# Optimization experiments

Measured on AMD Instinct MI355X. Metric: run time of the kernel, lower is better.

The kernel has to match this reference:

```python
import jax, jax.numpy as jnp
import numpy as np

BATCH = 2048
N = 2 * BATCH
TEMP = 0.5
BN_EPS = 1e-5
COS_EPS = 1e-8

# Precompute (constant) flat indices of the negative entries: all (i,j) with
# j != i and j != i +- BATCH. Each row has exactly N-2 negatives.
_mask = np.ones((N, N), dtype=bool)
np.fill_diagonal(_mask, False)
for _i in range(BATCH):
    _mask[_i, BATCH + _i] = False
    _mask[BATCH + _i, _i] = False
NEG_IDX = np.nonzero(_mask.reshape(-1))[0]  # (N*(N-2),)


def _projector(h, W1, gamma, beta, W2, b2):
    # Linear (no bias) -> BatchNorm1d (training-mode batch stats) -> ReLU -> Linear
    x = h @ W1.T                                   # (B, latent)
    mu = jnp.mean(x, axis=0)
    var = jnp.mean(jnp.square(x - mu), axis=0)     # biased var, as torch BN
    x = (x - mu) * jax.lax.rsqrt(var + BN_EPS) * gamma + beta
    x = jax.nn.relu(x)
    return x @ W2.T + b2                           # (B, proj)


def setup_inputs() -> dict:
    key = jax.random.key(0)
    ks = jax.random.split(key, 4)
    latent, proj = 2048, 256
    return {
        "h_i": jax.random.normal(ks[0], (BATCH, latent), jnp.float32),
        "h_j": jax.random.normal(ks[1], (BATCH, latent), jnp.float32),
        "W1": jax.random.normal(ks[2], (latent, latent), jnp.float32) / np.sqrt(latent),
        "gamma": jnp.ones((latent,), jnp.float32),
        "beta": jnp.zeros((latent,), jnp.float32),
        "W2": jax.random.normal(ks[3], (proj, latent), jnp.float32) / np.sqrt(latent),
        "b2": jnp.zeros((proj,), jnp.float32),
    }


def reference(h_i, h_j, W1, gamma, beta, W2, b2):
    z_i = _projector(h_i, W1, gamma, beta, W2, b2)
    z_j = _projector(h_j, W1, gamma, beta, W2, b2)
    z = jnp.concatenate([z_i, z_j], axis=0)                      # (N, proj)
    # cosine similarity: normalize once, then a single GEMM
    zn = z / jnp.maximum(jnp.linalg.norm(z, axis=1, keepdims=True), COS_EPS)
    sim = (zn @ zn.T) / TEMP                                     # (N, N)
    sim_i_j = jnp.diagonal(sim, offset=BATCH)                    # (BATCH,)
    sim_j_i = jnp.diagonal(sim, offset=-BATCH)                   # (BATCH,)
    positives = jnp.concatenate([sim_i_j, sim_j_i])[:, None]     # (N, 1)
    negatives = sim.reshape(-1)[NEG_IDX].reshape(N, N - 2)       # (N, N-2)
    logits = jnp.concatenate([positives, negatives], axis=1)     # (N, N-1)
    # cross-entropy with label 0 for every row, reduction='sum', then / N
    loss = jnp.sum(jax.nn.logsumexp(logits, axis=1) - logits[:, 0]) / N
    return loss
```

## Files before the change

### kernel.cpp

```cpp
#include <hip/hip_runtime.h>
#include <hip/hip_fp8.h>
#include <math.h>

#define BATCH   2048
#define NROWS   4096
#define LATENT  2048
#define PROJ    256
#define TEMP_INV 2.0f
#define BN_EPS  1e-5f
#define COS_EPS 1e-8f
#define W1SCALE 32.0f
#define W1INV   (1.0f / 32.0f)

typedef __bf16 bf16x8 __attribute__((ext_vector_type(8)));
typedef float  f32x4  __attribute__((ext_vector_type(4)));
typedef long   i64;

__device__ __forceinline__ unsigned short f2bf(float f) {
    union { float f; unsigned int u; } c; c.f = f;
    return (unsigned short)((c.u + 0x7FFFu + ((c.u >> 16) & 1u)) >> 16);
}
__device__ __forceinline__ float bf2f(unsigned short h) {
    union { unsigned int u; float f; } c; c.u = ((unsigned int)h) << 16;
    return c.f;
}
__device__ __forceinline__ unsigned char f2fp8(float f) {
    __hip_fp8_e4m3 t(f);
    return (unsigned char)t.__x;
}

__device__ __forceinline__ void gl_lds16(const void* g, void* l) {
    __builtin_amdgcn_global_load_lds(
        (const __attribute__((address_space(1))) void*)g,
        (__attribute__((address_space(3))) void*)l, 16, 0, 0);
}

__device__ __forceinline__ int swz(int R, int lk) {
    return R * 32 + ((lk ^ ((R >> 1) & 3)) << 3);
}
__device__ __forceinline__ int mix8(int R) {
    return (R & 7) ^ ((R >> 1) & 4);
}

#define G1 1048576
#define G2 2097152
#define G3 3145728
#define G4 3276800
__global__ __launch_bounds__(256) void cvt_all_kernel(
    const float* __restrict__ h_i, const float* __restrict__ h_j,
    const float* __restrict__ W1,  const float* __restrict__ W2,
    unsigned char* __restrict__ Hq, unsigned char* __restrict__ W1q,
    unsigned short* __restrict__ W2b)
{
    int i = blockIdx.x * 256 + threadIdx.x;
    if (i >= G4) return;
    if (i < G2) {
        const float* src = (i < G1) ? h_i : h_j;
        int off = (i < G1) ? i : i - G1;
        float4 v = reinterpret_cast<const float4*>(src)[off];
        uchar4 o;
        o.x = f2fp8(v.x); o.y = f2fp8(v.y); o.z = f2fp8(v.z); o.w = f2fp8(v.w);
        reinterpret_cast<uchar4*>(Hq)[i] = o;
    } else if (i < G3) {
        int off = i - G2;
        float4 v = reinterpret_cast<const float4*>(W1)[off];
        uchar4 o;
        o.x = f2fp8(v.x * W1SCALE); o.y = f2fp8(v.y * W1SCALE);
        o.z = f2fp8(v.z * W1SCALE); o.w = f2fp8(v.w * W1SCALE);
        reinterpret_cast<uchar4*>(W1q)[off] = o;
    } else {
        int off = i - G3;
        float4 v = reinterpret_cast<const float4*>(W2)[off];
        ushort4 o;
        o.x = f2bf(v.x); o.y = f2bf(v.y); o.z = f2bf(v.z); o.w = f2bf(v.w);
        reinterpret_cast<ushort4*>(W2b)[off] = o;
    }
}

template<int KSTRIDE, int KLEN, int WM, int WN>
__device__ __forceinline__ void mfma_loop(
    const unsigned short* __restrict__ Ab,
    const unsigned short* __restrict__ Bb,
    unsigned short* As, unsigned short* Bs,
    f32x4 acc[WM][WN], int tid)
{
    constexpr int BM = WM * 32;
    constexpr int BN = WN * 32;
    const int wid = tid >> 6, lane = tid & 63;
    const int mblk = (wid >> 1) * (WM * 16);
    const int nblk = (wid & 1) * (WN * 16);
    const int lr = lane & 15, lk = lane >> 4;
    for (int k0 = 0; k0 < KLEN; k0 += 32) {
        __syncthreads();
        #pragma unroll
        for (int u = 0; u < BM / 64; ++u) {
            int li = u * 256 + tid;
            int r = li >> 2, c = (li & 3) ^ ((li >> 3) & 3);
            gl_lds16(Ab + (size_t)r * KSTRIDE + k0 + c * 8, As + li * 8);
        }
        #pragma unroll
        for (int u = 0; u < BN / 64; ++u) {
            int li = u * 256 + tid;
            int r = li >> 2, c = (li & 3) ^ ((li >> 3) & 3);
            gl_lds16(Bb + (size_t)r * KSTRIDE + k0 + c * 8, Bs + li * 8);
        }
        __syncthreads();
        bf16x8 af[WM], bv[WN];
        #pragma unroll
        for (int i = 0; i < WM; ++i)
            af[i] = *reinterpret_cast<const bf16x8*>(As + swz(mblk + i * 16 + lr, lk));
        #pragma unroll
        for (int j = 0; j < WN; ++j)
            bv[j] = *reinterpret_cast<const bf16x8*>(Bs + swz(nblk + j * 16 + lr, lk));
        #pragma unroll
        for (int i = 0; i < WM; ++i)
            #pragma unroll
            for (int j = 0; j < WN; ++j)
                acc[i][j] = __builtin_amdgcn_mfma_f32_16x16x32_bf16(af[i], bv[j], acc[i][j], 0, 0, 0);
    }
}

__global__ __launch_bounds__(256, 4) void gemm1_fp8(
    const unsigned char* __restrict__ Hq, const unsigned char* __restrict__ W1q,
    unsigned short* __restrict__ Xb, float* __restrict__ sums, float* __restrict__ sumsqs)
{
    __shared__ __align__(16) unsigned char As[128 * 128];
    __shared__ __align__(16) unsigned char Bs[64 * 128];
    const int tid = threadIdx.x;
    const int m0 = blockIdx.y * 128, n0 = blockIdx.x * 64;
    const unsigned char* Ab = Hq + (size_t)m0 * LATENT;
    const unsigned char* Bb = W1q + (size_t)n0 * LATENT;
    const int wid = tid >> 6, lane = tid & 63;
    const int mblk = (wid >> 1) * 64, nblk = (wid & 1) * 32;
    const int lr = lane & 15, lk = lane >> 4;
    f32x4 zero = {0.f, 0.f, 0.f, 0.f};
    f32x4 acc[4][2];
    #pragma unroll
    for (int i = 0; i < 4; ++i) { acc[i][0] = zero; acc[i][1] = zero; }

    for (int k0 = 0; k0 < LATENT; k0 += 128) {
        __syncthreads();
        #pragma unroll
        for (int u = 0; u < 4; ++u) {
            int li = u * 256 + tid;
            int r = li >> 3, s = li & 7;
            gl_lds16(Ab + (size_t)r * LATENT + k0 + ((s ^ mix8(r)) * 16), As + li * 16);
        }
        #pragma unroll
        for (int u = 0; u < 2; ++u) {
            int li = u * 256 + tid;
            int r = li >> 3, s = li & 7;
            gl_lds16(Bb + (size_t)r * LATENT + k0 + ((s ^ mix8(r)) * 16), Bs + li * 16);
        }
        __syncthreads();
        i64 af[4][4], bv[2][4];
        #pragma unroll
        for (int i = 0; i < 4; ++i) {
            int R = mblk + i * 16 + lr;
            int mr = mix8(R);
            int base = R * 128 + (lk & 1) * 8;
            #pragma unroll
            for (int t = 0; t < 4; ++t) {
                int g = 2 * t + (lk >> 1);
                af[i][t] = *reinterpret_cast<const i64*>(As + base + ((g ^ mr) << 4));
            }
        }
        #pragma unroll
        for (int j = 0; j < 2; ++j) {
            int R = nblk + j * 16 + lr;
            int mr = mix8(R);
            int base = R * 128 + (lk & 1) * 8;
            #pragma unroll
            for (int t = 0; t < 4; ++t) {
                int g = 2 * t + (lk >> 1);
                bv[j][t] = *reinterpret_cast<const i64*>(Bs + base + ((g ^ mr) << 4));
            }
        }
        #pragma unroll
        for (int t = 0; t < 4; ++t)
            #pragma unroll
            for (int i = 0; i < 4; ++i)
                #pragma unroll
                for (int j = 0; j < 2; ++j)
                    acc[i][j] = __builtin_amdgcn_mfma_f32_16x16x32_fp8_fp8(
                        af[i][t], bv[j][t], acc[i][j], 0, 0, 0);
    }

    const int lq = lane >> 4;
    const int half = m0 >> 11;
    #pragma unroll
    for (int j = 0; j < 2; ++j) {
        float s = 0.f, q = 0.f;
        #pragma unroll
        for (int i = 0; i < 4; ++i)
            #pragma unroll
            for (int r = 0; r < 4; ++r) {
                float v = acc[i][j][r] * W1INV;
                s += v; q += v * v;
                int row = m0 + mblk + i * 16 + lq * 4 + r;
                int col = n0 + nblk + j * 16 + lr;
                Xb[(size_t)row * LATENT + col] = f2bf(v);
            }
        s += __shfl_xor(s, 16, 64);  q += __shfl_xor(q, 16, 64);
        s += __shfl_xor(s, 32, 64);  q += __shfl_xor(q, 32, 64);
        if (lq == 0) {
            int col = n0 + nblk + j * 16 + lr;
            atomicAdd(&sums[half * LATENT + col], s);
            atomicAdd(&sumsqs[half * LATENT + col], q);
        }
    }
}

__global__ __launch_bounds__(256) void gemm2_mfma(
    const unsigned short* __restrict__ Xb, const unsigned short* __restrict__ W2b,
    const float* __restrict__ sums, const float* __restrict__ sumsqs,
    const float* __restrict__ gamma, const float* __restrict__ beta,
    unsigned short* __restrict__ Zpb)
{
    __shared__ __align__(16) unsigned short As[128 * 32];
    __shared__ __align__(16) unsigned short Bs[64 * 32];
    __shared__ __align__(16) float scs[512];
    __shared__ __align__(16) float shs[512];
    const int tid = threadIdx.x;
    const int m0 = blockIdx.y * 128, n0 = blockIdx.x * 64, kc = blockIdx.z;
    const unsigned short* Ab = Xb + (size_t)m0 * LATENT + kc * 512;
    const unsigned short* Bb = W2b + (size_t)n0 * LATENT + kc * 512;
    const int half = m0 >> 11;
    #pragma unroll
    for (int u = 0; u < 2; ++u) {
        int e = u * 256 + tid;
        int col = kc * 512 + e;
        int g = half * LATENT + col;
        float mu  = sums[g] * (1.0f / BATCH);
        float var = sumsqs[g] * (1.0f / BATCH) - mu * mu;
        float sc = gamma[col] * rsqrtf(var + BN_EPS);
        scs[e] = sc;
        shs[e] = beta[col] - mu * sc;
    }
    const int wid = tid >> 6, lane = tid & 63;
    const int mblk = (wid >> 1) * 64, nblk = (wid & 1) * 32;
    const int lr = lane & 15, lk = lane >> 4;
    f32x4 zero = {0.f, 0.f, 0.f, 0.f};
    f32x4 acc[4][2];
    #pragma unroll
    for (int i = 0; i < 4; ++i) { acc[i][0] = zero; acc[i][1] = zero; }

    for (int k0 = 0; k0 < 512; k0 += 32) {
        __syncthreads();
        #pragma unroll
        for (int u = 0; u < 2; ++u) {
            int li = u * 256 + tid;
            int r = li >> 2, c = (li & 3) ^ ((li >> 3) & 3);
            gl_lds16(Ab + (size_t)r * LATENT + k0 + c * 8, As + li * 8);
        }
        {
            int li = tid;
            int r = li >> 2, c = (li & 3) ^ ((li >> 3) & 3);
            gl_lds16(Bb + (size_t)r * LATENT + k0 + c * 8, Bs + li * 8);
        }
        __syncthreads();
        float4 sc0 = *reinterpret_cast<const float4*>(scs + k0 + lk * 8);
        float4 sc1 = *reinterpret_cast<const float4*>(scs + k0 + lk * 8 + 4);
        float4 sh0 = *reinterpret_cast<const float4*>(shs + k0 + lk * 8);
        float4 sh1 = *reinterpret_cast<const float4*>(shs + k0 + lk * 8 + 4);
        bf16x8 af[4], bv[2];
        #pragma unroll
        for (int i = 0; i < 4; ++i) {
            bf16x8 raw = *reinterpret_cast<const bf16x8*>(As + swz(mblk + i * 16 + lr, lk));
            bf16x8 a;
            a[0] = (__bf16)fmaxf(fmaf((float)raw[0], sc0.x, sh0.x), 0.f);
            a[1] = (__bf16)fmaxf(fmaf((float)raw[1], sc0.y, sh0.y), 0.f);
            a[2] = (__bf16)fmaxf(fmaf((float)raw[2], sc0.z, sh0.z), 0.f);
            a[3] = (__bf16)fmaxf(fmaf((float)raw[3], sc0.w, sh0.w), 0.f);
            a[4] = (__bf16)fmaxf(fmaf((float)raw[4], sc1.x, sh1.x), 0.f);
            a[5] = (__bf16)fmaxf(fmaf((float)raw[5], sc1.y, sh1.y), 0.f);
            a[6] = (__bf16)fmaxf(fmaf((float)raw[6], sc1.z, sh1.z), 0.f);
            a[7] = (__bf16)fmaxf(fmaf((float)raw[7], sc1.w, sh1.w), 0.f);
            af[i] = a;
        }
        #pragma unroll
        for (int j = 0; j < 2; ++j)
            bv[j] = *reinterpret_cast<const bf16x8*>(Bs + swz(nblk + j * 16 + lr, lk));
        #pragma unroll
        for (int i = 0; i < 4; ++i)
            #pragma unroll
            for (int j = 0; j < 2; ++j)
                acc[i][j] = __builtin_amdgcn_mfma_f32_16x16x32_bf16(af[i], bv[j], acc[i][j], 0, 0, 0);
    }

    unsigned short* Zk = Zpb + (size_t)kc * NROWS * PROJ;
    const int lq = lane >> 4;
    #pragma unroll
    for (int i = 0; i < 4; ++i)
        #pragma unroll
        for (int j = 0; j < 2; ++j)
            #pragma unroll
            for (int r = 0; r < 4; ++r) {
                int row = m0 + mblk + i * 16 + lq * 4 + r;
                int col = n0 + nblk + j * 16 + lr;
                Zk[(size_t)row * PROJ + col] = f2bf(acc[i][j][r]);
            }
}

__global__ __launch_bounds__(256) void rownorm_kernel(
    const unsigned short* __restrict__ Zpb, const float* __restrict__ b2,
    unsigned short* __restrict__ ZNb)
{
    const int wave = threadIdx.x >> 6;
    const int lane = threadIdx.x & 63;
    const int row = blockIdx.x * 4 + wave;
    float v[4];
    float sq = 0.f;
    #pragma unroll
    for (int i = 0; i < 4; ++i) {
        int col = lane + i * 64;
        float t = b2[col];
        #pragma unroll
        for (int c = 0; c < 4; ++c)
            t += bf2f(Zpb[(size_t)c * NROWS * PROJ + (size_t)row * PROJ + col]);
        v[i] = t;
        sq += t * t;
    }
    #pragma unroll
    for (int off = 32; off > 0; off >>= 1) sq += __shfl_xor(sq, off, 64);
    float inv = 1.0f / fmaxf(sqrtf(sq), COS_EPS);
    #pragma unroll
    for (int i = 0; i < 4; ++i)
        ZNb[(size_t)row * PROJ + lane + i * 64] = f2bf(v[i] * inv);
}

__global__ __launch_bounds__(256) void simlse_mfma(
    const unsigned short* __restrict__ ZNb, float* __restrict__ rowsum,
    float* __restrict__ dgA, float* __restrict__ posA)
{
    if (blockIdx.x < blockIdx.y) return;
    __shared__ __align__(16) unsigned short As[128 * 32];
    __shared__ __align__(16) unsigned short Bs[128 * 32];
    const int tid = threadIdx.x;
    const int r0 = blockIdx.y * 128, j0 = blockIdx.x * 128;
    const bool offdiag = (j0 != r0);
    f32x4 zero = {0.f, 0.f, 0.f, 0.f};
    f32x4 acc[4][4];
    #pragma unroll
    for (int i = 0; i < 4; ++i)
        #pragma unroll
        for (int j = 0; j < 4; ++j) acc[i][j] = zero;
    mfma_loop<PROJ, PROJ, 4, 4>(ZNb + (size_t)r0 * PROJ, ZNb + (size_t)j0 * PROJ,
                                As, Bs, acc, tid);
    const int wid = tid >> 6, lane = tid & 63;
    const int mblk = (wid >> 1) * 64, nblk = (wid & 1) * 64;
    const int lr = lane & 15, lq = lane >> 4;
    float tcol[4] = {0.f, 0.f, 0.f, 0.f};
    #pragma unroll
    for (int i = 0; i < 4; ++i)
        #pragma unroll
        for (int r = 0; r < 4; ++r) {
            int R = r0 + mblk + i * 16 + lq * 4 + r;
            int P = (R < BATCH) ? R + BATCH : R - BATCH;
            float t = 0.f;
            #pragma unroll
            for (int j = 0; j < 4; ++j) {
                int J = j0 + nblk + j * 16 + lr;
                float s = acc[i][j][r] * TEMP_INV;
                float e = __expf(s);
                t += e;
                tcol[j] += e;
                if (J == R) dgA[R] = e;
                if (J == P) { posA[R] = s; posA[J] = s; }
            }
            t += __shfl_xor(t, 1, 64);
            t += __shfl_xor(t, 2, 64);
            t += __shfl_xor(t, 4, 64);
            t += __shfl_xor(t, 8, 64);
            if (lr == 0) atomicAdd(&rowsum[R], t);
        }
    if (offdiag) {
        #pragma unroll
        for (int j = 0; j < 4; ++j) {
            float c = tcol[j];
            c += __shfl_xor(c, 16, 64);
            c += __shfl_xor(c, 32, 64);
            if (lq == 0) atomicAdd(&rowsum[j0 + nblk + j * 16 + lr], c);
        }
    }
}

__global__ __launch_bounds__(256) void loss_kernel(
    const float* __restrict__ rowsum, const float* __restrict__ dgA,
    const float* __restrict__ posA, float* __restrict__ out)
{
    __shared__ float red[256];
    float s = 0.f;
    for (int r = threadIdx.x; r < NROWS; r += 256)
        s += logf(rowsum[r] - dgA[r]) - posA[r];
    red[threadIdx.x] = s;
    __syncthreads();
    for (int off = 128; off > 0; off >>= 1) {
        if (threadIdx.x < off) red[threadIdx.x] += red[threadIdx.x + off];
        __syncthreads();
    }
    if (threadIdx.x == 0) out[0] = red[0] * (1.0f / NROWS);
}

extern "C" void kernel_launch(void* const* d_in, const int* in_sizes, int n_in,
                              void* d_out, int out_size, void* d_ws, size_t ws_size,
                              hipStream_t stream)
{
    const float* h_i   = (const float*)d_in[0];
    const float* h_j   = (const float*)d_in[1];
    const float* W1    = (const float*)d_in[2];
    const float* gamma = (const float*)d_in[3];
    const float* beta  = (const float*)d_in[4];
    const float* W2    = (const float*)d_in[5];
    const float* b2    = (const float*)d_in[6];
    float* out = (float*)d_out;

    unsigned short* Zpb = (unsigned short*)d_ws;
    float* sums   = (float*)(Zpb + (size_t)4 * NROWS * PROJ);
    float* sumsqs = sums + 2 * LATENT;
    float* rowsum = sumsqs + 2 * LATENT;
    float* dgA    = rowsum + NROWS;
    float* posA   = dgA + NROWS;
    unsigned char* Hq  = (unsigned char*)(posA + NROWS);
    unsigned char* W1q = Hq + (size_t)NROWS * LATENT;
    unsigned short* W2b = (unsigned short*)(W1q + (size_t)LATENT * LATENT);
    unsigned short* Xb  = W2b + (size_t)PROJ * LATENT;
    unsigned short* ZNb = Xb + (size_t)NROWS * LATENT;

    hipMemsetAsync(sums, 0, (size_t)(4 * LATENT + NROWS) * sizeof(float), stream);

    cvt_all_kernel<<<(G4 + 255) / 256, 256, 0, stream>>>(h_i, h_j, W1, W2, Hq, W1q, W2b);
    gemm1_fp8<<<dim3(LATENT / 64, NROWS / 128), 256, 0, stream>>>(Hq, W1q, Xb, sums, sumsqs);
    gemm2_mfma<<<dim3(PROJ / 64, NROWS / 128, 4), 256, 0, stream>>>(Xb, W2b, sums, sumsqs, gamma, beta, Zpb);
    rownorm_kernel<<<NROWS / 4, 256, 0, stream>>>(Zpb, b2, ZNb);
    simlse_mfma<<<dim3(NROWS / 128, NROWS / 128), 256, 0, stream>>>(ZNb, rowsum, dgA, posA);
    loss_kernel<<<1, 256, 0, stream>>>(rowsum, dgA, posA, out);
}
```

Before: 176.0 us.

## Move projector second GEMM and similarity GEMM to FP8 MFMA

The hidden activations are stored as FP8 instead of BF16. BatchNorm+ReLU moves out of the GEMM2 inner loop into a separate in-place pass, and GEMM2 then runs on a shared FP8 MFMA loop with W2 quantized and scaled. The normalized embeddings are quantized to scaled FP8, and the similarity GEMM loads the full K=256 tile into LDS once and uses FP8 MFMA. The accumulator memset is folded into the conversion kernel. The aim is to halve operand bandwidth and raise MFMA throughput, at the cost of an extra elementwise pass and a loss of accuracy from FP8 rounding in the logits.

```diff
diff --git a/kernel.cpp b/kernel.cpp
--- a/kernel.cpp
+++ b/kernel.cpp
@@ -6,15 +6,15 @@
 #define NROWS   4096
 #define LATENT  2048
 #define PROJ    256
-#define TEMP_INV 2.0f
 #define BN_EPS  1e-5f
 #define COS_EPS 1e-8f
 #define W1SCALE 32.0f
 #define W1INV   (1.0f / 32.0f)
-
-typedef __bf16 bf16x8 __attribute__((ext_vector_type(8)));
-typedef float  f32x4  __attribute__((ext_vector_type(4)));
-typedef long   i64;
+#define ZNSCALE 16.0f
+#define SIMSCALE (1.0f / 128.0f)
+
+typedef float f32x4 __attribute__((ext_vector_type(4)));
+typedef long  i64;
 
 __device__ __forceinline__ unsigned short f2bf(float f) {
     union { float f; unsigned int u; } c; c.f = f;
@@ -27,6 +27,10 @@
 __device__ __forceinline__ unsigned char f2fp8(float f) {
     __hip_fp8_e4m3 t(f);
     return (unsigned char)t.__x;
+}
+__device__ __forceinline__ float fp82f(unsigned char b) {
+    __hip_fp8_e4m3 t; t.__x = b;
+    return (float)t;
 }
 
 __device__ __forceinline__ void gl_lds16(const void* g, void* l) {
@@ -35,9 +39,6 @@
         (__attribute__((address_space(3))) void*)l, 16, 0, 0);
 }
 
-__device__ __forceinline__ int swz(int R, int lk) {
-    return R * 32 + ((lk ^ ((R >> 1) & 3)) << 3);
-}
 __device__ __forceinline__ int mix8(int R) {
     return (R & 7) ^ ((R >> 1) & 4);
 }
@@ -50,9 +51,13 @@
     const float* __restrict__ h_i, const float* __restrict__ h_j,
     const float* __restrict__ W1,  const float* __restrict__ W2,
     unsigned char* __restrict__ Hq, unsigned char* __restrict__ W1q,
-    unsigned short* __restrict__ W2b)
+    unsigned char* __restrict__ W2q, float* __restrict__ zeroacc)
 {
     int i = blockIdx.x * 256 + threadIdx.x;
+    if (blockIdx.x == 0) {
+        #pragma unroll
+        for (int u = 0; u < 48; ++u) zeroacc[u * 256 + threadIdx.x] = 0.f;
+    }
     if (i >= G4) return;
     if (i < G2) {
         const float* src = (i < G1) ? h_i : h_j;
@@ -71,86 +76,34 @@
     } else {
         int off = i - G3;
         float4 v = reinterpret_cast<const float4*>(W2)[off];
-        ushort4 o;
-        o.x = f2bf(v.x); o.y = f2bf(v.y); o.z = f2bf(v.z); o.w = f2bf(v.w);
-        reinterpret_cast<ushort4*>(W2b)[off] = o;
-    }
-}
-
-template<int KSTRIDE, int KLEN, int WM, int WN>
-__device__ __forceinline__ void mfma_loop(
-    const unsigned short* __restrict__ Ab,
-    const unsigned short* __restrict__ Bb,
-    unsigned short* As, unsigned short* Bs,
-    f32x4 acc[WM][WN], int tid)
-{
-    constexpr int BM = WM * 32;
-    constexpr int BN = WN * 32;
-    const int wid = tid >> 6, lane = tid & 63;
-    const int mblk = (wid >> 1) * (WM * 16);
-    const int nblk = (wid & 1) * (WN * 16);
-    const int lr = lane & 15, lk = lane >> 4;
-    for (int k0 = 0; k0 < KLEN; k0 += 32) {
-        __syncthreads();
-        #pragma unroll
-        for (int u = 0; u < BM / 64; ++u) {
-            int li = u * 256 + tid;
-            int r = li >> 2, c = (li & 3) ^ ((li >> 3) & 3);
-            gl_lds16(Ab + (size_t)r * KSTRIDE + k0 + c * 8, As + li * 8);
-        }
-        #pragma unroll
-        for (int u = 0; u < BN / 64; ++u) {
-            int li = u * 256 + tid;
-            int r = li >> 2, c = (li & 3) ^ ((li >> 3) & 3);
-            gl_lds16(Bb + (size_t)r * KSTRIDE + k0 + c * 8, Bs + li * 8);
-        }
-        __syncthreads();
-        bf16x8 af[WM], bv[WN];
-        #pragma unroll
-        for (int i = 0; i < WM; ++i)
-            af[i] = *reinterpret_cast<const bf16x8*>(As + swz(mblk + i * 16 + lr, lk));
-        #pragma unroll
-        for (int j = 0; j < WN; ++j)
-            bv[j] = *reinterpret_cast<const bf16x8*>(Bs + swz(nblk + j * 16 + lr, lk));
-        #pragma unroll
-        for (int i = 0; i < WM; ++i)
-            #pragma unroll
-            for (int j = 0; j < WN; ++j)
-                acc[i][j] = __builtin_amdgcn_mfma_f32_16x16x32_bf16(af[i], bv[j], acc[i][j], 0, 0, 0);
-    }
-}
-
-__global__ __launch_bounds__(256, 4) void gemm1_fp8(
-    const unsigned char* __restrict__ Hq, const unsigned char* __restrict__ W1q,
-    unsigned short* __restrict__ Xb, float* __restrict__ sums, float* __restrict__ sumsqs)
-{
-    __shared__ __align__(16) unsigned char As[128 * 128];
-    __shared__ __align__(16) unsigned char Bs[64 * 128];
-    const int tid = threadIdx.x;
-    const int m0 = blockIdx.y * 128, n0 = blockIdx.x * 64;
-    const unsigned char* Ab = Hq + (size_t)m0 * LATENT;
-    const unsigned char* Bb = W1q + (size_t)n0 * LATENT;
+        uchar4 o;
+        o.x = f2fp8(v.x * W1SCALE); o.y = f2fp8(v.y * W1SCALE);
+        o.z = f2fp8(v.z * W1SCALE); o.w = f2fp8(v.w * W1SCALE);
+        reinterpret_cast<uchar4*>(W2q)[off] = o;
+    }
+}
+
+template<int KSTRIDE, int KLEN>
+__device__ __forceinline__ void fp8_loop(
+    const unsigned char* __restrict__ Ab, const unsigned char* __restrict__ Bb,
+    unsigned char* As, unsigned char* Bs, f32x4 acc[4][2], int tid)
+{
     const int wid = tid >> 6, lane = tid & 63;
     const int mblk = (wid >> 1) * 64, nblk = (wid & 1) * 32;
     const int lr = lane & 15, lk = lane >> 4;
-    f32x4 zero = {0.f, 0.f, 0.f, 0.f};
-    f32x4 acc[4][2];
-    #pragma unroll
-    for (int i = 0; i < 4; ++i) { acc[i][0] = zero; acc[i][1] = zero; }
-
-    for (int k0 = 0; k0 < LATENT; k0 += 128) {
+    for (int k0 = 0; k0 < KLEN; k0 += 128) {
         __syncthreads();
         #pragma unroll
         for (int u = 0; u < 4; ++u) {
             int li = u * 256 + tid;
             int r = li >> 3, s = li & 7;
-            gl_lds16(Ab + (size_t)r * LATENT + k0 + ((s ^ mix8(r)) * 16), As + li * 16);
+            gl_lds16(Ab + (size_t)r * KSTRIDE + k0 + ((s ^ mix8(r)) * 16), As + li * 16);
         }
         #pragma unroll
         for (int u = 0; u < 2; ++u) {
             int li = u * 256 + tid;
             int r = li >> 3, s = li & 7;
-            gl_lds16(Bb + (size_t)r * LATENT + k0 + ((s ^ mix8(r)) * 16), Bs + li * 16);
+            gl_lds16(Bb + (size_t)r * KSTRIDE + k0 + ((s ^ mix8(r)) * 16), Bs + li * 16);
         }
         __syncthreads();
         i64 af[4][4], bv[2][4];
@@ -185,8 +138,25 @@
                     acc[i][j] = __builtin_amdgcn_mfma_f32_16x16x32_fp8_fp8(
                         af[i][t], bv[j][t], acc[i][j], 0, 0, 0);
     }
-
-    const int lq = lane >> 4;
+}
+
+__global__ __launch_bounds__(256, 4) void gemm1_fp8(
+    const unsigned char* __restrict__ Hq, const unsigned char* __restrict__ W1q,
+    unsigned char* __restrict__ Xq, float* __restrict__ sums, float* __restrict__ sumsqs)
+{
+    __shared__ __align__(16) unsigned char As[128 * 128];
+    __shared__ __align__(16) unsigned char Bs[64 * 128];
+    const int tid = threadIdx.x;
+    const int m0 = blockIdx.y * 128, n0 = blockIdx.x * 64;
+    f32x4 zero = {0.f, 0.f, 0.f, 0.f};
+    f32x4 acc[4][2];
+    #pragma unroll
+    for (int i = 0; i < 4; ++i) { acc[i][0] = zero; acc[i][1] = zero; }
+    fp8_loop<LATENT, LATENT>(Hq + (size_t)m0 * LATENT, W1q + (size_t)n0 * LATENT,
+                             As, Bs, acc, tid);
+    const int wid = tid >> 6, lane = tid & 63;
+    const int mblk = (wid >> 1) * 64, nblk = (wid & 1) * 32;
+    const int lr = lane & 15, lq = lane >> 4;
     const int half = m0 >> 11;
     #pragma unroll
     for (int j = 0; j < 2; ++j) {
@@ -199,7 +169,7 @@
                 s += v; q += v * v;
                 int row = m0 + mblk + i * 16 + lq * 4 + r;
                 int col = n0 + nblk + j * 16 + lr;
-                Xb[(size_t)row * LATENT + col] = f2bf(v);
+                Xq[(size_t)row * LATENT + col] = f2fp8(v);
             }
         s += __shfl_xor(s, 16, 64);  q += __shfl_xor(q, 16, 64);
         s += __shfl_xor(s, 32, 64);  q += __shfl_xor(q, 32, 64);
@@ -211,85 +181,52 @@
     }
 }
 
-__global__ __launch_bounds__(256) void gemm2_mfma(
-    const unsigned short* __restrict__ Xb, const unsigned short* __restrict__ W2b,
-    const float* __restrict__ sums, const float* __restrict__ sumsqs,
-    const float* __restrict__ gamma, const float* __restrict__ beta,
+__global__ __launch_bounds__(256) void bnrelu8_kernel(
+    unsigned char* __restrict__ Xq, const float* __restrict__ sums,
+    const float* __restrict__ sumsqs, const float* __restrict__ gamma,
+    const float* __restrict__ beta)
+{
+    const int row = blockIdx.x;
+    const int half = row >> 11;
+    const int col = threadIdx.x * 8;
+    size_t idx = (size_t)row * LATENT + col;
+    uchar4 a = *reinterpret_cast<const uchar4*>(Xq + idx);
+    uchar4 b = *reinterpret_cast<const uchar4*>(Xq + idx + 4);
+    uchar4 oa, ob;
+    #pragma unroll
+    for (int u = 0; u < 8; ++u) {
+        int c = col + u;
+        int g = half * LATENT + c;
+        float mu  = sums[g] * (1.0f / BATCH);
+        float var = sumsqs[g] * (1.0f / BATCH) - mu * mu;
+        float sc = gamma[c] * rsqrtf(var + BN_EPS);
+        float sh = beta[c] - mu * sc;
+        unsigned char x = (u < 4) ? ((const unsigned char*)&a)[u] : ((const unsigned char*)&b)[u - 4];
+        unsigned char o = f2fp8(fmaxf(fmaf(fp82f(x), sc, sh), 0.f));
+        if (u < 4) ((unsigned char*)&oa)[u] = o; else ((unsigned char*)&ob)[u - 4] = o;
+    }
+    *reinterpret_cast<uchar4*>(Xq + idx) = oa;
+    *reinterpret_cast<uchar4*>(Xq + idx + 4) = ob;
+}
+
+__global__ __launch_bounds__(256, 4) void gemm2_fp8(
+    const unsigned char* __restrict__ Xq, const unsigned char* __restrict__ W2q,
     unsigned short* __restrict__ Zpb)
 {
-    __shared__ __align__(16) unsigned short As[128 * 32];
-    __shared__ __align__(16) unsigned short Bs[64 * 32];
-    __shared__ __align__(16) float scs[512];
-    __shared__ __align__(16) float shs[512];
+    __shared__ __align__(16) unsigned char As[128 * 128];
+    __shared__ __align__(16) unsigned char Bs[64 * 128];
     const int tid = threadIdx.x;
     const int m0 = blockIdx.y * 128, n0 = blockIdx.x * 64, kc = blockIdx.z;
-    const unsigned short* Ab = Xb + (size_t)m0 * LATENT + kc * 512;
-    const unsigned short* Bb = W2b + (size_t)n0 * LATENT + kc * 512;
-    const int half = m0 >> 11;
-    #pragma unroll
-    for (int u = 0; u < 2; ++u) {
-        int e = u * 256 + tid;
-        int col = kc * 512 + e;
-        int g = half * LATENT + col;
-        float mu  = sums[g] * (1.0f / BATCH);
-        float var = sumsqs[g] * (1.0f / BATCH) - mu * mu;
-        float sc = gamma[col] * rsqrtf(var + BN_EPS);
-        scs[e] = sc;
-        shs[e] = beta[col] - mu * sc;
-    }
+    f32x4 zero = {0.f, 0.f, 0.f, 0.f};
+    f32x4 acc[4][2];
+    #pragma unroll
+    for (int i = 0; i < 4; ++i) { acc[i][0] = zero; acc[i][1] = zero; }
+    fp8_loop<LATENT, 512>(Xq + (size_t)m0 * LATENT + kc * 512,
+                          W2q + (size_t)n0 * LATENT + kc * 512, As, Bs, acc, tid);
+    unsigned short* Zk = Zpb + (size_t)kc * NROWS * PROJ;
     const int wid = tid >> 6, lane = tid & 63;
     const int mblk = (wid >> 1) * 64, nblk = (wid & 1) * 32;
-    const int lr = lane & 15, lk = lane >> 4;
-    f32x4 zero = {0.f, 0.f, 0.f, 0.f};
-    f32x4 acc[4][2];
-    #pragma unroll
-    for (int i = 0; i < 4; ++i) { acc[i][0] = zero; acc[i][1] = zero; }
-
-    for (int k0 = 0; k0 < 512; k0 += 32) {
-        __syncthreads();
-        #pragma unroll
-        for (int u = 0; u < 2; ++u) {
-            int li = u * 256 + tid;
-            int r = li >> 2, c = (li & 3) ^ ((li >> 3) & 3);
-            gl_lds16(Ab + (size_t)r * LATENT + k0 + c * 8, As + li * 8);
-        }
-        {
-            int li = tid;
-            int r = li >> 2, c = (li & 3) ^ ((li >> 3) & 3);
-            gl_lds16(Bb + (size_t)r * LATENT + k0 + c * 8, Bs + li * 8);
-        }
-        __syncthreads();
-        float4 sc0 = *reinterpret_cast<const float4*>(scs + k0 + lk * 8);
-        float4 sc1 = *reinterpret_cast<const float4*>(scs + k0 + lk * 8 + 4);
-        float4 sh0 = *reinterpret_cast<const float4*>(shs + k0 + lk * 8);
-        float4 sh1 = *reinterpret_cast<const float4*>(shs + k0 + lk * 8 + 4);
-        bf16x8 af[4], bv[2];
-        #pragma unroll
-        for (int i = 0; i < 4; ++i) {
-            bf16x8 raw = *reinterpret_cast<const bf16x8*>(As + swz(mblk + i * 16 + lr, lk));
-            bf16x8 a;
-            a[0] = (__bf16)fmaxf(fmaf((float)raw[0], sc0.x, sh0.x), 0.f);
-            a[1] = (__bf16)fmaxf(fmaf((float)raw[1], sc0.y, sh0.y), 0.f);
-            a[2] = (__bf16)fmaxf(fmaf((float)raw[2], sc0.z, sh0.z), 0.f);
-            a[3] = (__bf16)fmaxf(fmaf((float)raw[3], sc0.w, sh0.w), 0.f);
-            a[4] = (__bf16)fmaxf(fmaf((float)raw[4], sc1.x, sh1.x), 0.f);
-            a[5] = (__bf16)fmaxf(fmaf((float)raw[5], sc1.y, sh1.y), 0.f);
-            a[6] = (__bf16)fmaxf(fmaf((float)raw[6], sc1.z, sh1.z), 0.f);
-            a[7] = (__bf16)fmaxf(fmaf((float)raw[7], sc1.w, sh1.w), 0.f);
-            af[i] = a;
-        }
-        #pragma unroll
-        for (int j = 0; j < 2; ++j)
-            bv[j] = *reinterpret_cast<const bf16x8*>(Bs + swz(nblk + j * 16 + lr, lk));
-        #pragma unroll
-        for (int i = 0; i < 4; ++i)
-            #pragma unroll
-            for (int j = 0; j < 2; ++j)
-                acc[i][j] = __builtin_amdgcn_mfma_f32_16x16x32_bf16(af[i], bv[j], acc[i][j], 0, 0, 0);
-    }
-
-    unsigned short* Zk = Zpb + (size_t)kc * NROWS * PROJ;
-    const int lq = lane >> 4;
+    const int lr = lane & 15, lq = lane >> 4;
     #pragma unroll
     for (int i = 0; i < 4; ++i)
         #pragma unroll
@@ -298,13 +235,13 @@
             for (int r = 0; r < 4; ++r) {
                 int row = m0 + mblk + i * 16 + lq * 4 + r;
                 int col = n0 + nblk + j * 16 + lr;
-                Zk[(size_t)row * PROJ + col] = f2bf(acc[i][j][r]);
+                Zk[(size_t)row * PROJ + col] = f2bf(acc[i][j][r] * W1INV);
             }
 }
 
 __global__ __launch_bounds__(256) void rownorm_kernel(
     const unsigned short* __restrict__ Zpb, const float* __restrict__ b2,
-    unsigned short* __restrict__ ZNb)
+    unsigned char* __restrict__ ZNq)
 {
     const int wave = threadIdx.x >> 6;
     const int lane = threadIdx.x & 63;
@@ -323,33 +260,69 @@
     }
     #pragma unroll
     for (int off = 32; off > 0; off >>= 1) sq += __shfl_xor(sq, off, 64);
-    float inv = 1.0f / fmaxf(sqrtf(sq), COS_EPS);
+    float inv = ZNSCALE / fmaxf(sqrtf(sq), COS_EPS);
     #pragma unroll
     for (int i = 0; i < 4; ++i)
-        ZNb[(size_t)row * PROJ + lane + i * 64] = f2bf(v[i] * inv);
-}
-
-__global__ __launch_bounds__(256) void simlse_mfma(
-    const unsigned short* __restrict__ ZNb, float* __restrict__ rowsum,
+        ZNq[(size_t)row * PROJ + lane + i * 64] = f2fp8(v[i] * inv);
+}
+
+__global__ __launch_bounds__(256) void simlse_fp8(
+    const unsigned char* __restrict__ ZNq, float* __restrict__ rowsum,
     float* __restrict__ dgA, float* __restrict__ posA)
 {
     if (blockIdx.x < blockIdx.y) return;
-    __shared__ __align__(16) unsigned short As[128 * 32];
-    __shared__ __align__(16) unsigned short Bs[128 * 32];
+    __shared__ __align__(16) unsigned char As[128 * 256];
+    __shared__ __align__(16) unsigned char Bs[128 * 256];
     const int tid = threadIdx.x;
     const int r0 = blockIdx.y * 128, j0 = blockIdx.x * 128;
     const bool offdiag = (j0 != r0);
+    const unsigned char* Ab = ZNq + (size_t)r0 * PROJ;
+    const unsigned char* Bb = ZNq + (size_t)j0 * PROJ;
+    #pragma unroll
+    for (int u = 0; u < 8; ++u) {
+        int li = u * 256 + tid;
+        int r = li >> 4, s = li & 15;
+        int c = s ^ (r & 15);
+        gl_lds16(Ab + (size_t)r * PROJ + c * 16, As + li * 16);
+    }
+    #pragma unroll
+    for (int u = 0; u < 8; ++u) {
+        int li = u * 256 + tid;
+        int r = li >> 4, s = li & 15;
+        int c = s ^ (r & 15);
+        gl_lds16(Bb + (size_t)r * PROJ + c * 16, Bs + li * 16);
+    }
+    __syncthreads();
+    const int wid = tid >> 6, lane = tid & 63;
+    const int mblk = (wid >> 1) * 64, nblk = (wid & 1) * 64;
+    const int lr = lane & 15, lk = lane >> 4;
     f32x4 zero = {0.f, 0.f, 0.f, 0.f};
     f32x4 acc[4][4];
     #pragma unroll
     for (int i = 0; i < 4; ++i)
         #pragma unroll
         for (int j = 0; j < 4; ++j) acc[i][j] = zero;
-    mfma_loop<PROJ, PROJ, 4, 4>(ZNb + (size_t)r0 * PROJ, ZNb + (size_t)j0 * PROJ,
-                                As, Bs, acc, tid);
-    const int wid = tid >> 6, lane = tid & 63;
-    const int mblk = (wid >> 1) * 64, nblk = (wid & 1) * 64;
-    const int lr = lane & 15, lq = lane >> 4;
+    #pragma unroll
+    for (int t = 0; t < 8; ++t) {
+        int g = 2 * t + (lk >> 1);
+        i64 af[4], bv[4];
+        #pragma unroll
+        for (int i = 0; i < 4; ++i) {
+            int R = mblk + i * 16 + lr;
+            af[i] = *reinterpret_cast<const i64*>(As + R * 256 + ((g ^ (R & 15)) << 4) + (lk & 1) * 8);
+        }
+        #pragma unroll
+        for (int j = 0; j < 4; ++j) {
+            int R = nblk + j * 16 + lr;
+            bv[j] = *reinterpret_cast<const i64*>(Bs + R * 256 + ((g ^ (R & 15)) << 4) + (lk & 1) * 8);
+        }
+        #pragma unroll
+        for (int i = 0; i < 4; ++i)
+            #pragma unroll
+            for (int j = 0; j < 4; ++j)
+                acc[i][j] = __builtin_amdgcn_mfma_f32_16x16x32_fp8_fp8(af[i], bv[j], acc[i][j], 0, 0, 0);
+    }
+    const int lq = lane >> 4;
     float tcol[4] = {0.f, 0.f, 0.f, 0.f};
     #pragma unroll
     for (int i = 0; i < 4; ++i)
@@ -361,7 +334,7 @@
             #pragma unroll
             for (int j = 0; j < 4; ++j) {
                 int J = j0 + nblk + j * 16 + lr;
-                float s = acc[i][j][r] * TEMP_INV;
+                float s = acc[i][j][r] * SIMSCALE;
                 float e = __expf(s);
                 t += e;
                 tcol[j] += e;
@@ -423,16 +396,15 @@
     float* posA   = dgA + NROWS;
     unsigned char* Hq  = (unsigned char*)(posA + NROWS);
     unsigned char* W1q = Hq + (size_t)NROWS * LATENT;
-    unsigned short* W2b = (unsigned short*)(W1q + (size_t)LATENT * LATENT);
-    unsigned short* Xb  = W2b + (size_t)PROJ * LATENT;
-    unsigned short* ZNb = Xb + (size_t)NROWS * LATENT;
-
-    hipMemsetAsync(sums, 0, (size_t)(4 * LATENT + NROWS) * sizeof(float), stream);
-
-    cvt_all_kernel<<<(G4 + 255) / 256, 256, 0, stream>>>(h_i, h_j, W1, W2, Hq, W1q, W2b);
-    gemm1_fp8<<<dim3(LATENT / 64, NROWS / 128), 256, 0, stream>>>(Hq, W1q, Xb, sums, sumsqs);
-    gemm2_mfma<<<dim3(PROJ / 64, NROWS / 128, 4), 256, 0, stream>>>(Xb, W2b, sums, sumsqs, gamma, beta, Zpb);
-    rownorm_kernel<<<NROWS / 4, 256, 0, stream>>>(Zpb, b2, ZNb);
-    simlse_mfma<<<dim3(NROWS / 128, NROWS / 128), 256, 0, stream>>>(ZNb, rowsum, dgA, posA);
+    unsigned char* W2q = W1q + (size_t)LATENT * LATENT;
+    unsigned char* Xq  = W2q + (size_t)PROJ * LATENT;
+    unsigned char* ZNq = Xq + (size_t)NROWS * LATENT;
+
+    cvt_all_kernel<<<(G4 + 255) / 256, 256, 0, stream>>>(h_i, h_j, W1, W2, Hq, W1q, W2q, sums);
+    gemm1_fp8<<<dim3(LATENT / 64, NROWS / 128), 256, 0, stream>>>(Hq, W1q, Xq, sums, sumsqs);
+    bnrelu8_kernel<<<NROWS, 256, 0, stream>>>(Xq, sums, sumsqs, gamma, beta);
+    gemm2_fp8<<<dim3(PROJ / 64, NROWS / 128, 4), 256, 0, stream>>>(Xq, W2q, Zpb);
+    rownorm_kernel<<<NROWS / 4, 256, 0, stream>>>(Zpb, b2, ZNq);
+    simlse_fp8<<<dim3(NROWS / 128, NROWS / 128), 256, 0, stream>>>(ZNq, rowsum, dgA, posA);
     loss_kernel<<<1, 256, 0, stream>>>(rowsum, dgA, posA, out);
 }
```

New measurement: 173.3 us. About the same (-1.6%).
